# Optimization experiments

Hardware: AMD Instinct MI355X
Metric: run time of the kernel (lower is better)

The kernel has to match this reference:

```python
import jax, jax.numpy as jnp
import numpy as np

RATIO, NH, NG, KS, RF, UP = 4, 2, 2, 3, 11.0, 2


def _cln(t, g, b):
    # channel-wise LayerNorm on NCHW (LayerNormProxy), eps=1e-5
    mu = t.mean(axis=1, keepdims=True)
    var = ((t - mu) ** 2).mean(axis=1, keepdims=True)
    return (t - mu) * jax.lax.rsqrt(var + 1e-5) * g[None, :, None, None] + b[None, :, None, None]


def _resize_ac(img, oH, oW):
    # bilinear resize, align_corners=True (F.interpolate)
    H, W = img.shape[-2], img.shape[-1]
    ys = jnp.arange(oH, dtype=img.dtype) * ((H - 1) / (oH - 1))
    y0 = jnp.clip(jnp.floor(ys), 0, H - 2).astype(jnp.int32)
    wy = ys - y0.astype(img.dtype)
    xs = jnp.arange(oW, dtype=img.dtype) * ((W - 1) / (oW - 1))
    x0 = jnp.clip(jnp.floor(xs), 0, W - 2).astype(jnp.int32)
    wx = xs - x0.astype(img.dtype)
    t = img[..., y0, :] * (1.0 - wy)[:, None] + img[..., y0 + 1, :] * wy[:, None]
    return t[..., x0] * (1.0 - wx) + t[..., x0 + 1] * wx


def _grid_sample(img, iy, ix):
    # bilinear grid_sample, padding_mode='zeros', align_corners=True
    # img [Bg,Cx,H,W]; iy,ix [Bg,N] unnormalized input-pixel coords
    H, W = img.shape[-2], img.shape[-1]
    def one(im, yy, xx):
        y0f, x0f = jnp.floor(yy), jnp.floor(xx)
        wy, wx = yy - y0f, xx - x0f
        y0, x0 = y0f.astype(jnp.int32), x0f.astype(jnp.int32)
        def gat(yi, xi):
            valid = ((yi >= 0) & (yi < H) & (xi >= 0) & (xi < W)).astype(im.dtype)
            return im[:, jnp.clip(yi, 0, H - 1), jnp.clip(xi, 0, W - 1)] * valid[None]
        return (gat(y0, x0) * ((1 - wy) * (1 - wx))[None]
                + gat(y0, x0 + 1) * ((1 - wy) * wx)[None]
                + gat(y0 + 1, x0) * (wy * (1 - wx))[None]
                + gat(y0 + 1, x0 + 1) * (wy * wx)[None])
    return jax.vmap(one)(img, iy, ix)


def _conv2d(x, w, groups=1):
    return jax.lax.conv_general_dilated(x, w, (1, 1), 'SAME', feature_group_count=groups,
                                        dimension_numbers=('NCHW', 'OIHW', 'NCHW'))


def _forward(x, ln_g, ln_b, Wq, Wk, dw_w, off_ln_g, off_ln_b, off_w, off_b, rpb):
    B, C, H, W = x.shape
    hidden = C // RATIO
    gc = hidden // NG
    c2 = hidden // NH          # attn_dim per head
    oH, oW = int(H * UP), int(W * UP)
    N1, n = oH * oW, KS * KS
    scale = c2 ** -0.5
    v = x
    xn = _cln(x, ln_g, ln_b)
    q = jnp.einsum('oc,bchw->bohw', Wq, xn)
    k = jnp.einsum('oc,bchw->bohw', Wk, xn)
    q = _resize_ac(q, oH, oW)                        # [B,hidden,oH,oW]
    # offset prediction
    q_off = q.reshape(B * NG, gc, oH, oW)
    t = _conv2d(q_off, dw_w, groups=gc)
    t = _cln(t, off_ln_g, off_ln_b)
    t = jax.nn.gelu(t, approximate=False)
    pred = _conv2d(t, off_w) + off_b[None, :, None, None]  # [Bg,2*ks^2,oH,oW]
    pad = (KS - 1) // 2
    rng = jnp.arange(-pad, pad + 1, dtype=x.dtype)
    base = jnp.stack(jnp.meshgrid(rng, rng, indexing='ij'), axis=-1)  # [KS,KS,2] (y,x)
    off = jnp.tanh(pred).reshape(B * NG, KS, KS, 2, oH, oW) * RF + base[None, :, :, :, None, None]
    py = off[:, :, :, 0] + jnp.arange(oH, dtype=x.dtype)[None, None, None, :, None]
    px = off[:, :, :, 1] + jnp.arange(oW, dtype=x.dtype)[None, None, None, None, :]
    # normalize over (oH-1,oW-1) then denormalize onto (H-1,W-1) input grid (align_corners)
    iy = (py * ((H - 1) / (oH - 1))).reshape(B * NG, -1)
    ix = (px * ((W - 1) / (oW - 1))).reshape(B * NG, -1)
    kg = k.reshape(B * NG, hidden // NG, H, W)
    vg = v.reshape(B * NG, C // NG, H, W)
    kf = _grid_sample(kg, iy, ix).reshape(B, NG, hidden // NG, n, oH, oW)
    vf = _grid_sample(vg, iy, ix).reshape(B, NG, C // NG, n, oH, oW)
    # -> [B, N1, n, g*c] -> [B, nh, N1, n, c]
    kf = kf.transpose(0, 4, 5, 3, 1, 2).reshape(B, N1, n, NH, hidden // NH).transpose(0, 3, 1, 2, 4)
    vf = vf.transpose(0, 4, 5, 3, 1, 2).reshape(B, N1, n, NH, C // NH).transpose(0, 3, 1, 2, 4)
    kf = kf + rpb                                     # relative position bias on K
    qh = q.reshape(B, NH, c2, N1).transpose(0, 1, 3, 2) * scale  # [B,nh,N1,c2]
    attn = jax.nn.softmax(jnp.einsum('bhnc,bhnkc->bhnk', qh, kf), axis=-1)
    out = jnp.einsum('bhnk,bhnkc->bhnc', attn, vf)    # [B,nh,N1,C/nh]
    return out.transpose(0, 1, 3, 2).reshape(B, C, oH, oW)


def setup_inputs() -> dict:
    key = jax.random.key(0)
    ks = jax.random.split(key, 8)
    B, C, H, W = 2, 256, 48, 48
    hidden = C // RATIO
    gc = hidden // NG
    c2 = hidden // NH
    f32 = jnp.float32
    return {
        'x': jax.random.normal(ks[0], (B, C, H, W), f32),
        'ln_g': jnp.ones((C,), f32),
        'ln_b': jnp.zeros((C,), f32),
        'Wq': jax.random.normal(ks[1], (hidden, C), f32) * 0.05,
        'Wk': jax.random.normal(ks[2], (hidden, C), f32) * 0.05,
        'dw_w': jax.random.normal(ks[3], (gc, 1, 3, 3), f32) * 0.1,
        'off_ln_g': jnp.ones((gc,), f32),
        'off_ln_b': jnp.zeros((gc,), f32),
        'off_w': jax.random.normal(ks[4], (2 * KS * KS, gc, 3, 3), f32) * 0.02,
        'off_b': jnp.zeros((2 * KS * KS,), f32),
        'rpb': jax.random.normal(ks[5], (1, NH, 1, KS * KS, c2), f32) * 0.02,
    }


def reference(x, ln_g, ln_b, Wq, Wk, dw_w, off_ln_g, off_ln_b, off_w, off_b, rpb):
    return _forward(x, ln_g, ln_b, Wq, Wk, dw_w, off_ln_g, off_ln_b, off_w, off_b, rpb)
```

## Files before the change

### kernel.cpp

```cpp
#include <hip/hip_runtime.h>
#include <cstdint>
#include <cmath>

#define NB 2
#define NC 256
#define HW 2304
#define HID 64
#define OH 96
#define OW 96
#define N1 9216
#define SCALE_ATTN 0.17677669529663689f
#define RESZ ((float)(47.0/95.0))

__global__ void kA_prep(const float* __restrict__ x, const float* __restrict__ Wq,
                        const float* __restrict__ Wk, const float* __restrict__ off_w,
                        float* __restrict__ v_nhwc, float* __restrict__ WT4,
                        float* __restrict__ wT2) {
    int blk = blockIdx.x;
    if (blk < 1152) {
        int pt = blk % 72;
        int t2 = blk / 72;
        int ct = t2 & 3;
        int bg = t2 >> 2;
        int b = bg >> 1, g = bg & 1;
        __shared__ float tile[32][33];
        int tx = threadIdx.x & 31, row = threadIdx.x >> 5;
#pragma unroll
        for (int r = 0; r < 4; r++) {
            int c = ct * 32 + row + r * 8;
            tile[row + r * 8][tx] = x[((size_t)(b * 256 + g * 128 + c)) * HW + pt * 32 + tx];
        }
        __syncthreads();
#pragma unroll
        for (int r = 0; r < 4; r++) {
            int p = pt * 32 + row + r * 8;
            v_nhwc[((size_t)bg * HW + p) * 128 + ct * 32 + tx] = tile[tx][row + r * 8];
        }
    } else {
        int idx = (blk - 1152) * 256 + threadIdx.x;
        if (idx < 256 * 128) {
            int c = idx >> 7, t = idx & 127;
            float v = (t < 64) ? Wq[t * 256 + c] : Wk[(t - 64) * 256 + c];
            WT4[(((size_t)(c >> 2) * 128) + t) * 4 + (c & 3)] = v;
        } else if (idx < 256 * 128 + 288 * 18) {
            int i = idx - 256 * 128;
            wT2[i] = off_w[(i % 18) * 288 + (i / 18)];
        }
    }
}

__global__ __launch_bounds__(256) void k1_ln_qk(const float* __restrict__ v_nhwc,
                         const float* __restrict__ ln_g, const float* __restrict__ ln_b,
                         const float* __restrict__ WT4,
                         float* __restrict__ q_pix, float* __restrict__ k_nhwc) {
    int blk = blockIdx.x;
    int tid = threadIdx.x;
    int wv = tid >> 6, lane = tid & 63;
    __shared__ float xs[4][256];
    {
        int pix = blk * 4 + wv;
        int b = pix / HW, p = pix % HW;
        int c0 = lane * 2;
        float2 u0 = *(const float2*)(v_nhwc + (((size_t)(b * 2 + 0) * HW) + p) * 128 + c0);
        float2 u1 = *(const float2*)(v_nhwc + (((size_t)(b * 2 + 1) * HW) + p) * 128 + c0);
        float s = u0.x + u0.y + u1.x + u1.y;
#pragma unroll
        for (int off = 1; off < 64; off <<= 1) s += __shfl_xor(s, off);
        float mu = s * (1.f / 256.f);
        float d0 = u0.x - mu, d1 = u0.y - mu, d2 = u1.x - mu, d3 = u1.y - mu;
        float q = d0 * d0 + d1 * d1 + d2 * d2 + d3 * d3;
#pragma unroll
        for (int off = 1; off < 64; off <<= 1) q += __shfl_xor(q, off);
        float rs = rsqrtf(q * (1.f / 256.f) + 1e-5f);
        float2 w0, w1;
        w0.x = d0 * rs * ln_g[c0] + ln_b[c0];
        w0.y = d1 * rs * ln_g[c0 + 1] + ln_b[c0 + 1];
        w1.x = d2 * rs * ln_g[128 + c0] + ln_b[128 + c0];
        w1.y = d3 * rs * ln_g[129 + c0] + ln_b[129 + c0];
        *(float2*)&xs[wv][c0] = w0;
        *(float2*)&xs[wv][128 + c0] = w1;
    }
    __syncthreads();
    int o = tid & 127, ph = tid >> 7;
    float a0 = 0.f, a1 = 0.f;
    const float4* wp = (const float4*)WT4 + o;
    const float4* xa = (const float4*)xs[ph * 2];
    const float4* xb = (const float4*)xs[ph * 2 + 1];
#pragma unroll 8
    for (int c4 = 0; c4 < 64; c4++) {
        float4 w = wp[(size_t)c4 * 128];
        float4 p0 = xa[c4], p1 = xb[c4];
        a0 += w.x * p0.x + w.y * p0.y + w.z * p0.z + w.w * p0.w;
        a1 += w.x * p1.x + w.y * p1.y + w.z * p1.z + w.w * p1.w;
    }
#pragma unroll
    for (int k = 0; k < 2; k++) {
        int pix = blk * 4 + ph * 2 + k;
        int b = pix / HW, p = pix % HW;
        float a = k ? a1 : a0;
        if (o < 64) {
            q_pix[(((size_t)b * HW) + p) * 64 + o] = a;
        } else {
            int t = o - 64, g = t >> 5, c32 = t & 31;
            k_nhwc[(((size_t)(b * 2 + g) * HW) + p) * 32 + c32] = a;
        }
    }
}

__global__ __launch_bounds__(256) void k34_off(const float* __restrict__ q_pix,
                                               const float* __restrict__ dw_w,
                                               const float* __restrict__ og,
                                               const float* __restrict__ ob,
                                               const float* __restrict__ wT2,
                                               const float* __restrict__ off_b,
                                               float* __restrict__ pred) {
    int blk = blockIdx.x;
    int bg = blk / 72, tile = blk % 72;
    int ty0 = (tile / 6) * 8, tx0 = (tile % 6) * 16;
    int b = bg >> 1, g = bg & 1;
    int tid = threadIdx.x;
    __shared__ float ts[180][33];

    if (tid < 180) {
        int hy = ty0 + tid / 18 - 1;
        int hx = tx0 + tid % 18 - 1;
        if (hy < 0 || hy >= OH || hx < 0 || hx >= OW) {
#pragma unroll
            for (int c = 0; c < 32; c++) ts[tid][c] = 0.f;
        } else {
            const float* qb = q_pix + (size_t)b * HW * 64 + g * 32;
            float vals[32];
#pragma unroll
            for (int c = 0; c < 32; c++) vals[c] = 0.f;
            for (int dy = -1; dy <= 1; dy++) {
                int yy = hy + dy;
                if ((unsigned)yy >= (unsigned)OH) continue;
                float ysf = yy * RESZ;
                int y0 = min((int)ysf, 46);
                float wy = ysf - (float)y0;
                for (int dx = -1; dx <= 1; dx++) {
                    int xx = hx + dx;
                    if ((unsigned)xx >= (unsigned)OW) continue;
                    float xsf = xx * RESZ;
                    int x0 = min((int)xsf, 46);
                    float wx = xsf - (float)x0;
                    int i00 = (y0 * 48 + x0) * 64;
                    const float4* q00 = (const float4*)(qb + i00);
                    const float4* q01 = (const float4*)(qb + i00 + 64);
                    const float4* q10 = (const float4*)(qb + i00 + 48 * 64);
                    const float4* q11 = (const float4*)(qb + i00 + 49 * 64);
                    float w00 = (1.f - wy) * (1.f - wx), w01 = (1.f - wy) * wx;
                    float w10 = wy * (1.f - wx),         w11 = wy * wx;
                    int wi = (dy + 1) * 3 + (dx + 1);
#pragma unroll
                    for (int c4 = 0; c4 < 8; c4++) {
                        float4 a = q00[c4], bq = q01[c4], cq = q10[c4], dq = q11[c4];
                        float qx = w00 * a.x + w01 * bq.x + w10 * cq.x + w11 * dq.x;
                        float qy = w00 * a.y + w01 * bq.y + w10 * cq.y + w11 * dq.y;
                        float qz = w00 * a.z + w01 * bq.z + w10 * cq.z + w11 * dq.z;
                        float qw = w00 * a.w + w01 * bq.w + w10 * cq.w + w11 * dq.w;
                        vals[c4 * 4 + 0] += qx * dw_w[(c4 * 4 + 0) * 9 + wi];
                        vals[c4 * 4 + 1] += qy * dw_w[(c4 * 4 + 1) * 9 + wi];
                        vals[c4 * 4 + 2] += qz * dw_w[(c4 * 4 + 2) * 9 + wi];
                        vals[c4 * 4 + 3] += qw * dw_w[(c4 * 4 + 3) * 9 + wi];
                    }
                }
            }
            float sum = 0.f;
#pragma unroll
            for (int c = 0; c < 32; c++) sum += vals[c];
            float mu = sum * (1.f / 32.f);
            float var = 0.f;
#pragma unroll
            for (int c = 0; c < 32; c++) { float d = vals[c] - mu; var += d * d; }
            float rsv = rsqrtf(var * (1.f / 32.f) + 1e-5f);
#pragma unroll
            for (int c = 0; c < 32; c++) {
                float v = (vals[c] - mu) * rsv * og[c] + ob[c];
                ts[tid][c] = 0.5f * v * (1.f + erff(v * 0.70710678118654752f));
            }
        }
    }
    __syncthreads();

    int och = __builtin_amdgcn_readfirstlane(tid >> 7) * 9;
    int pixL = tid & 127;
    int oyl = pixL >> 4, oxl = pixL & 15;
    float acc[9];
#pragma unroll
    for (int o = 0; o < 9; o++) acc[o] = off_b[och + o];
    for (int ic = 0; ic < 32; ic++) {
#pragma unroll
        for (int dy = 0; dy < 3; dy++) {
#pragma unroll
            for (int dx = 0; dx < 3; dx++) {
                float tv = ts[(oyl + dy) * 18 + oxl + dx][ic];
                const float* wr = wT2 + (ic * 9 + dy * 3 + dx) * 18 + och;
#pragma unroll
                for (int o = 0; o < 9; o++) acc[o] += tv * wr[o];
            }
        }
    }
    int p = (ty0 + oyl) * OW + tx0 + oxl;
#pragma unroll
    for (int o = 0; o < 9; o++)
        pred[((size_t)bg * 18 + och + o) * N1 + p] = acc[o];
}

__global__ __launch_bounds__(256) void k5_attn(const float* __restrict__ pred,
                                               const float* __restrict__ q_pix,
                                               const float* __restrict__ k_nhwc,
                                               const float* __restrict__ v_nhwc,
                                               const float* __restrict__ rpb,
                                               float* __restrict__ out) {
    int tid = threadIdx.x;
    int wv = __builtin_amdgcn_readfirstlane(tid >> 6);
    int lane = tid & 63;
    int gp = blockIdx.x * 16;
    int bg = gp / N1, p0 = gp % N1;
    int b = bg >> 1, g = bg & 1;
    int pw = p0 + wv * 4;
    int oy = pw / OW, ox0 = pw % OW;

    __shared__ float4 wts[4][4][9];
    __shared__ int4   cof[4][4][9];
    __shared__ float  outb[4][4][128];

    if (lane < 36) {
        int px = lane / 9, j = lane % 9;
        int p = pw + px;
        int ky = j / 3, kx = j % 3;
        float pr0 = pred[((size_t)bg * 18 + j * 2) * N1 + p];
        float pr1 = pred[((size_t)bg * 18 + j * 2 + 1) * N1 + p];
        float th0 = 1.f - 2.f * __builtin_amdgcn_rcpf(__expf(2.f * pr0) + 1.f);
        float th1 = 1.f - 2.f * __builtin_amdgcn_rcpf(__expf(2.f * pr1) + 1.f);
        float py  = th0 * 11.0f + (float)(ky - 1) + (float)oy;
        float pxc = th1 * 11.0f + (float)(kx - 1) + (float)(ox0 + px);
        float iy = py * RESZ, ix = pxc * RESZ;
        float y0f = floorf(iy), x0f = floorf(ix);
        float wy = iy - y0f, wx = ix - x0f;
        int y0 = (int)y0f, x0 = (int)x0f;
        bool vy0 = (unsigned)y0 < 48u, vy1 = (unsigned)(y0 + 1) < 48u;
        bool vx0 = (unsigned)x0 < 48u, vx1 = (unsigned)(x0 + 1) < 48u;
        int y0c = min(max(y0, 0), 47), y1c = min(max(y0 + 1, 0), 47);
        int x0c = min(max(x0, 0), 47), x1c = min(max(x0 + 1, 0), 47);
        float4 w;
        w.x = (vy0 && vx0) ? (1.f - wy) * (1.f - wx) : 0.f;
        w.y = (vy0 && vx1) ? (1.f - wy) * wx : 0.f;
        w.z = (vy1 && vx0) ? wy * (1.f - wx) : 0.f;
        w.w = (vy1 && vx1) ? wy * wx : 0.f;
        wts[wv][px][j] = w;
        cof[wv][px][j] = make_int4(y0c * 48 + x0c, y0c * 48 + x1c,
                                   y1c * 48 + x0c, y1c * 48 + x1c);
    }
    __syncthreads();

    int c = lane & 31, h = lane >> 5;
    int c4 = (lane & 31) * 4;
    const float* kb = k_nhwc + (size_t)bg * HW * 32;
    const float* rb = rpb + (size_t)g * 288;
    const float* qb = q_pix + (size_t)b * HW * 64 + g * 32 + c;
    const float* vbase = v_nhwc + (size_t)bg * HW * 128;

    float ysf = oy * RESZ;
    int qy0 = min((int)ysf, 46);
    float qwy = ysf - (float)qy0;

    for (int px = 0; px < 4; px++) {
        float xsf = (ox0 + px) * RESZ;
        int qx0 = min((int)xsf, 46);
        float qwx = xsf - (float)qx0;
        int qi = (qy0 * 48 + qx0) * 64;
        float q00 = qb[qi], q01 = qb[qi + 64];
        float q10 = qb[qi + 48 * 64], q11 = qb[qi + 49 * 64];
        float qv = ((q00 * (1.f - qwy) + q10 * qwy) * (1.f - qwx)
                  + (q01 * (1.f - qwy) + q11 * qwy) * qwx) * SCALE_ATTN;

        float s[5], e[5];
#pragma unroll
        for (int jj = 0; jj < 5; jj++) {
            int j = jj * 2 + h;
            float partial = 0.f;
            if (j < 9) {
                float4 w = wts[wv][px][j];
                int4 co = cof[wv][px][j];
                float kv = w.x * kb[co.x * 32 + c] + w.y * kb[co.y * 32 + c]
                         + w.z * kb[co.z * 32 + c] + w.w * kb[co.w * 32 + c];
                partial = qv * (kv + rb[j * 32 + c]);
            }
#pragma unroll
            for (int off = 1; off < 32; off <<= 1) partial += __shfl_xor(partial, off);
            s[jj] = (j < 9) ? partial : -1e30f;
        }
        float m = s[0];
#pragma unroll
        for (int jj = 1; jj < 5; jj++) m = fmaxf(m, s[jj]);
        m = fmaxf(m, __shfl_xor(m, 32));
        float sum = 0.f;
#pragma unroll
        for (int jj = 0; jj < 5; jj++) { e[jj] = __expf(s[jj] - m); sum += e[jj]; }
        sum += __shfl_xor(sum, 32);
        float inv = __builtin_amdgcn_rcpf(sum);

        float4 acc = make_float4(0.f, 0.f, 0.f, 0.f);
#pragma unroll
        for (int jj = 0; jj < 5; jj++) {
            int j = jj * 2 + h;
            if (j < 9) {
                float pj = e[jj] * inv;
                float4 w = wts[wv][px][j];
                int4 co = cof[wv][px][j];
                float4 a0 = *(const float4*)(vbase + (size_t)co.x * 128 + c4);
                float4 a1 = *(const float4*)(vbase + (size_t)co.y * 128 + c4);
                float4 a2 = *(const float4*)(vbase + (size_t)co.z * 128 + c4);
                float4 a3 = *(const float4*)(vbase + (size_t)co.w * 128 + c4);
                float f0 = w.x * pj, f1 = w.y * pj, f2 = w.z * pj, f3 = w.w * pj;
                acc.x += f0 * a0.x + f1 * a1.x + f2 * a2.x + f3 * a3.x;
                acc.y += f0 * a0.y + f1 * a1.y + f2 * a2.y + f3 * a3.y;
                acc.z += f0 * a0.z + f1 * a1.z + f2 * a2.z + f3 * a3.z;
                acc.w += f0 * a0.w + f1 * a1.w + f2 * a2.w + f3 * a3.w;
            }
        }
        acc.x += __shfl_xor(acc.x, 32);
        acc.y += __shfl_xor(acc.y, 32);
        acc.z += __shfl_xor(acc.z, 32);
        acc.w += __shfl_xor(acc.w, 32);
        if (lane < 32) *(float4*)&outb[wv][px][c4] = acc;
    }
    __syncthreads();

    if (tid < 128) {
        int ch = tid;
        float* op = out + ((size_t)b * NC + g * 128 + ch) * N1 + p0;
#pragma unroll
        for (int w2 = 0; w2 < 4; w2++) {
            float4 v4 = make_float4(outb[w2][0][ch], outb[w2][1][ch],
                                    outb[w2][2][ch], outb[w2][3][ch]);
            *(float4*)(op + w2 * 4) = v4;
        }
    }
}

extern "C" void kernel_launch(void* const* d_in, const int* in_sizes, int n_in,
                              void* d_out, int out_size, void* d_ws, size_t ws_size,
                              hipStream_t stream) {
    const float* x      = (const float*)d_in[0];
    const float* ln_g   = (const float*)d_in[1];
    const float* ln_b   = (const float*)d_in[2];
    const float* Wq     = (const float*)d_in[3];
    const float* Wk     = (const float*)d_in[4];
    const float* dw_w   = (const float*)d_in[5];
    const float* off_g  = (const float*)d_in[6];
    const float* off_bt = (const float*)d_in[7];
    const float* off_w  = (const float*)d_in[8];
    const float* off_b  = (const float*)d_in[9];
    const float* rpb    = (const float*)d_in[10];
    float* out = (float*)d_out;

    float* ws = (float*)d_ws;
    float* WT4    = ws;
    float* k_nhwc = WT4 + 32768;
    float* v_nhwc = k_nhwc + 294912;
    float* q_pix  = v_nhwc + 1179648;
    float* pred   = q_pix + 294912;
    float* wT2    = pred + 663552;

    kA_prep<<<1301, 256, 0, stream>>>(x, Wq, Wk, off_w, v_nhwc, WT4, wT2);
    k1_ln_qk<<<1152, 256, 0, stream>>>(v_nhwc, ln_g, ln_b, WT4, q_pix, k_nhwc);
    k34_off<<<288, 256, 0, stream>>>(q_pix, dw_w, off_g, off_bt, wT2, off_b, pred);
    k5_attn<<<2304, 256, 0, stream>>>(pred, q_pix, k_nhwc, v_nhwc, rpb, out);
}
```

Baseline: 187.4 us.

## Split offset-network kernel into per-channel and per-output-channel kernels, reorder transpose

The fused k34_off kernel, which had only 288 blocks and heavy per-thread register arrays, is replaced by two high-parallelism kernels. k3_t computes the upsampled depthwise conv, LayerNorm and GELU with one thread per channel per pixel, using wave shuffles for the reductions. k4_pred computes the 3x3 offset conv with one thread per output channel per pixel, writing pred in pixel-major layout. The QK LayerNorm now reads x directly in NCHW instead of the transposed copy, and the v transpose runs later so it can reuse the buffer that held tbuf. This is meant to raise occupancy and parallelism at the cost of an extra intermediate buffer round trip through global memory and more redundant neighbour reads in k4.

```diff
diff --git a/kernel.cpp b/kernel.cpp
--- a/kernel.cpp
+++ b/kernel.cpp
@@ -12,44 +12,26 @@
 #define SCALE_ATTN 0.17677669529663689f
 #define RESZ ((float)(47.0/95.0))
 
-__global__ void kA_prep(const float* __restrict__ x, const float* __restrict__ Wq,
-                        const float* __restrict__ Wk, const float* __restrict__ off_w,
-                        float* __restrict__ v_nhwc, float* __restrict__ WT4,
-                        float* __restrict__ wT2) {
-    int blk = blockIdx.x;
-    if (blk < 1152) {
-        int pt = blk % 72;
-        int t2 = blk / 72;
-        int ct = t2 & 3;
-        int bg = t2 >> 2;
-        int b = bg >> 1, g = bg & 1;
-        __shared__ float tile[32][33];
-        int tx = threadIdx.x & 31, row = threadIdx.x >> 5;
-#pragma unroll
-        for (int r = 0; r < 4; r++) {
-            int c = ct * 32 + row + r * 8;
-            tile[row + r * 8][tx] = x[((size_t)(b * 256 + g * 128 + c)) * HW + pt * 32 + tx];
-        }
-        __syncthreads();
-#pragma unroll
-        for (int r = 0; r < 4; r++) {
-            int p = pt * 32 + row + r * 8;
-            v_nhwc[((size_t)bg * HW + p) * 128 + ct * 32 + tx] = tile[tx][row + r * 8];
-        }
-    } else {
-        int idx = (blk - 1152) * 256 + threadIdx.x;
-        if (idx < 256 * 128) {
-            int c = idx >> 7, t = idx & 127;
-            float v = (t < 64) ? Wq[t * 256 + c] : Wk[(t - 64) * 256 + c];
-            WT4[(((size_t)(c >> 2) * 128) + t) * 4 + (c & 3)] = v;
-        } else if (idx < 256 * 128 + 288 * 18) {
-            int i = idx - 256 * 128;
-            wT2[i] = off_w[(i % 18) * 288 + (i / 18)];
-        }
-    }
-}
-
-__global__ __launch_bounds__(256) void k1_ln_qk(const float* __restrict__ v_nhwc,
+__global__ void kA_prep(const float* __restrict__ Wq, const float* __restrict__ Wk,
+                        const float* __restrict__ off_w, const float* __restrict__ dw_w,
+                        float* __restrict__ WT4, float* __restrict__ wT2,
+                        float* __restrict__ dwT) {
+    int idx = blockIdx.x * 256 + threadIdx.x;
+    if (idx < 256 * 128) {
+        int c = idx >> 7, t = idx & 127;
+        float v = (t < 64) ? Wq[t * 256 + c] : Wk[(t - 64) * 256 + c];
+        WT4[(((size_t)(c >> 2) * 128) + t) * 4 + (c & 3)] = v;
+    } else if (idx < 256 * 128 + 288 * 18) {
+        int i = idx - 256 * 128;
+        wT2[i] = off_w[(i % 18) * 288 + (i / 18)];
+    } else if (idx < 256 * 128 + 288 * 18 + 288) {
+        int i = idx - (256 * 128 + 288 * 18);
+        int wi = i >> 5, c = i & 31;
+        dwT[i] = dw_w[c * 9 + wi];
+    }
+}
+
+__global__ __launch_bounds__(256) void k1_ln_qk(const float* __restrict__ x,
                          const float* __restrict__ ln_g, const float* __restrict__ ln_b,
                          const float* __restrict__ WT4,
                          float* __restrict__ q_pix, float* __restrict__ k_nhwc) {
@@ -59,44 +41,43 @@
     __shared__ float xs[4][256];
     {
         int pix = blk * 4 + wv;
-        int b = pix / HW, p = pix % HW;
-        int c0 = lane * 2;
-        float2 u0 = *(const float2*)(v_nhwc + (((size_t)(b * 2 + 0) * HW) + p) * 128 + c0);
-        float2 u1 = *(const float2*)(v_nhwc + (((size_t)(b * 2 + 1) * HW) + p) * 128 + c0);
-        float s = u0.x + u0.y + u1.x + u1.y;
+        int b = pix / HW, p = pix - b * HW;
+        const float* xb = x + (size_t)b * NC * HW + p;
+        float v0 = xb[(size_t)lane * HW];
+        float v1 = xb[(size_t)(lane + 64) * HW];
+        float v2 = xb[(size_t)(lane + 128) * HW];
+        float v3 = xb[(size_t)(lane + 192) * HW];
+        float s = v0 + v1 + v2 + v3;
 #pragma unroll
         for (int off = 1; off < 64; off <<= 1) s += __shfl_xor(s, off);
         float mu = s * (1.f / 256.f);
-        float d0 = u0.x - mu, d1 = u0.y - mu, d2 = u1.x - mu, d3 = u1.y - mu;
+        float d0 = v0 - mu, d1 = v1 - mu, d2 = v2 - mu, d3 = v3 - mu;
         float q = d0 * d0 + d1 * d1 + d2 * d2 + d3 * d3;
 #pragma unroll
         for (int off = 1; off < 64; off <<= 1) q += __shfl_xor(q, off);
         float rs = rsqrtf(q * (1.f / 256.f) + 1e-5f);
-        float2 w0, w1;
-        w0.x = d0 * rs * ln_g[c0] + ln_b[c0];
-        w0.y = d1 * rs * ln_g[c0 + 1] + ln_b[c0 + 1];
-        w1.x = d2 * rs * ln_g[128 + c0] + ln_b[128 + c0];
-        w1.y = d3 * rs * ln_g[129 + c0] + ln_b[129 + c0];
-        *(float2*)&xs[wv][c0] = w0;
-        *(float2*)&xs[wv][128 + c0] = w1;
+        xs[wv][lane]       = d0 * rs * ln_g[lane]       + ln_b[lane];
+        xs[wv][lane + 64]  = d1 * rs * ln_g[lane + 64]  + ln_b[lane + 64];
+        xs[wv][lane + 128] = d2 * rs * ln_g[lane + 128] + ln_b[lane + 128];
+        xs[wv][lane + 192] = d3 * rs * ln_g[lane + 192] + ln_b[lane + 192];
     }
     __syncthreads();
     int o = tid & 127, ph = tid >> 7;
     float a0 = 0.f, a1 = 0.f;
     const float4* wp = (const float4*)WT4 + o;
     const float4* xa = (const float4*)xs[ph * 2];
-    const float4* xb = (const float4*)xs[ph * 2 + 1];
+    const float4* xb4 = (const float4*)xs[ph * 2 + 1];
 #pragma unroll 8
     for (int c4 = 0; c4 < 64; c4++) {
         float4 w = wp[(size_t)c4 * 128];
-        float4 p0 = xa[c4], p1 = xb[c4];
+        float4 p0 = xa[c4], p1 = xb4[c4];
         a0 += w.x * p0.x + w.y * p0.y + w.z * p0.z + w.w * p0.w;
         a1 += w.x * p1.x + w.y * p1.y + w.z * p1.z + w.w * p1.w;
     }
 #pragma unroll
     for (int k = 0; k < 2; k++) {
         int pix = blk * 4 + ph * 2 + k;
-        int b = pix / HW, p = pix % HW;
+        int b = pix / HW, p = pix - b * HW;
         float a = k ? a1 : a0;
         if (o < 64) {
             q_pix[(((size_t)b * HW) + p) * 64 + o] = a;
@@ -107,104 +88,105 @@
     }
 }
 
-__global__ __launch_bounds__(256) void k34_off(const float* __restrict__ q_pix,
-                                               const float* __restrict__ dw_w,
-                                               const float* __restrict__ og,
-                                               const float* __restrict__ ob,
+__global__ __launch_bounds__(256) void k3_t(const float* __restrict__ q_pix,
+                                            const float* __restrict__ dwT,
+                                            const float* __restrict__ og,
+                                            const float* __restrict__ ob,
+                                            float* __restrict__ tbuf) {
+    int gid = blockIdx.x * 256 + threadIdx.x;
+    int c = gid & 31;
+    int p2 = gid >> 5;
+    int bg = p2 / N1, p = p2 - bg * N1;
+    int b = bg >> 1, g = bg & 1;
+    int oy = p / OW, ox = p - oy * OW;
+    const float* qb = q_pix + ((size_t)b * HW) * 64 + g * 32 + c;
+    float acc = 0.f;
+#pragma unroll
+    for (int dy = -1; dy <= 1; dy++) {
+        int yy = oy + dy;
+        if ((unsigned)yy >= (unsigned)OH) continue;
+        float ysf = yy * RESZ;
+        int y0 = min((int)ysf, 46);
+        float wy = ysf - (float)y0;
+#pragma unroll
+        for (int dx = -1; dx <= 1; dx++) {
+            int xx = ox + dx;
+            if ((unsigned)xx >= (unsigned)OW) continue;
+            float xsf = xx * RESZ;
+            int x0 = min((int)xsf, 46);
+            float wx = xsf - (float)x0;
+            int i00 = (y0 * 48 + x0) * 64;
+            float q00 = qb[i00], q01 = qb[i00 + 64];
+            float q10 = qb[i00 + 48 * 64], q11 = qb[i00 + 49 * 64];
+            float qv = (q00 * (1.f - wy) + q10 * wy) * (1.f - wx)
+                     + (q01 * (1.f - wy) + q11 * wy) * wx;
+            acc += qv * dwT[((dy + 1) * 3 + dx + 1) * 32 + c];
+        }
+    }
+    float s = acc;
+#pragma unroll
+    for (int off = 1; off < 32; off <<= 1) s += __shfl_xor(s, off);
+    float mu = s * (1.f / 32.f);
+    float d = acc - mu;
+    float v = d * d;
+#pragma unroll
+    for (int off = 1; off < 32; off <<= 1) v += __shfl_xor(v, off);
+    float rsv = rsqrtf(v * (1.f / 32.f) + 1e-5f);
+    float t = d * rsv * og[c] + ob[c];
+    float ge = 0.5f * t * (1.f + erff(t * 0.70710678118654752f));
+    tbuf[(size_t)p2 * 32 + c] = ge;
+}
+
+__global__ __launch_bounds__(256) void k4_pred(const float* __restrict__ tbuf,
                                                const float* __restrict__ wT2,
                                                const float* __restrict__ off_b,
                                                float* __restrict__ pred) {
+    int gid = blockIdx.x * 256 + threadIdx.x;
+    if (gid >= 4 * N1 * 18) return;
+    int p18 = gid / 18, oc = gid - p18 * 18;
+    int bg = p18 / N1, p = p18 - bg * N1;
+    int oy = p / OW, ox = p - oy * OW;
+    const float* tb = tbuf + (size_t)bg * N1 * 32;
+    int pn[9];
+    bool vl[9];
+#pragma unroll
+    for (int dy = -1; dy <= 1; dy++)
+#pragma unroll
+        for (int dx = -1; dx <= 1; dx++) {
+            int k = (dy + 1) * 3 + (dx + 1);
+            vl[k] = ((unsigned)(oy + dy) < (unsigned)OH) && ((unsigned)(ox + dx) < (unsigned)OW);
+            pn[k] = (p + dy * OW + dx) * 32;
+        }
+    float acc = off_b[oc];
+    for (int ic = 0; ic < 32; ic++) {
+#pragma unroll
+        for (int k = 0; k < 9; k++) {
+            if (vl[k]) acc += tb[pn[k] + ic] * wT2[(ic * 9 + k) * 18 + oc];
+        }
+    }
+    pred[gid] = acc;
+}
+
+__global__ void k2b_vt(const float* __restrict__ x, float* __restrict__ v_nhwc) {
     int blk = blockIdx.x;
-    int bg = blk / 72, tile = blk % 72;
-    int ty0 = (tile / 6) * 8, tx0 = (tile % 6) * 16;
+    int pt = blk % 72;
+    int t2 = blk / 72;
+    int ct = t2 & 3;
+    int bg = t2 >> 2;
     int b = bg >> 1, g = bg & 1;
-    int tid = threadIdx.x;
-    __shared__ float ts[180][33];
-
-    if (tid < 180) {
-        int hy = ty0 + tid / 18 - 1;
-        int hx = tx0 + tid % 18 - 1;
-        if (hy < 0 || hy >= OH || hx < 0 || hx >= OW) {
-#pragma unroll
-            for (int c = 0; c < 32; c++) ts[tid][c] = 0.f;
-        } else {
-            const float* qb = q_pix + (size_t)b * HW * 64 + g * 32;
-            float vals[32];
-#pragma unroll
-            for (int c = 0; c < 32; c++) vals[c] = 0.f;
-            for (int dy = -1; dy <= 1; dy++) {
-                int yy = hy + dy;
-                if ((unsigned)yy >= (unsigned)OH) continue;
-                float ysf = yy * RESZ;
-                int y0 = min((int)ysf, 46);
-                float wy = ysf - (float)y0;
-                for (int dx = -1; dx <= 1; dx++) {
-                    int xx = hx + dx;
-                    if ((unsigned)xx >= (unsigned)OW) continue;
-                    float xsf = xx * RESZ;
-                    int x0 = min((int)xsf, 46);
-                    float wx = xsf - (float)x0;
-                    int i00 = (y0 * 48 + x0) * 64;
-                    const float4* q00 = (const float4*)(qb + i00);
-                    const float4* q01 = (const float4*)(qb + i00 + 64);
-                    const float4* q10 = (const float4*)(qb + i00 + 48 * 64);
-                    const float4* q11 = (const float4*)(qb + i00 + 49 * 64);
-                    float w00 = (1.f - wy) * (1.f - wx), w01 = (1.f - wy) * wx;
-                    float w10 = wy * (1.f - wx),         w11 = wy * wx;
-                    int wi = (dy + 1) * 3 + (dx + 1);
-#pragma unroll
-                    for (int c4 = 0; c4 < 8; c4++) {
-                        float4 a = q00[c4], bq = q01[c4], cq = q10[c4], dq = q11[c4];
-                        float qx = w00 * a.x + w01 * bq.x + w10 * cq.x + w11 * dq.x;
-                        float qy = w00 * a.y + w01 * bq.y + w10 * cq.y + w11 * dq.y;
-                        float qz = w00 * a.z + w01 * bq.z + w10 * cq.z + w11 * dq.z;
-                        float qw = w00 * a.w + w01 * bq.w + w10 * cq.w + w11 * dq.w;
-                        vals[c4 * 4 + 0] += qx * dw_w[(c4 * 4 + 0) * 9 + wi];
-                        vals[c4 * 4 + 1] += qy * dw_w[(c4 * 4 + 1) * 9 + wi];
-                        vals[c4 * 4 + 2] += qz * dw_w[(c4 * 4 + 2) * 9 + wi];
-                        vals[c4 * 4 + 3] += qw * dw_w[(c4 * 4 + 3) * 9 + wi];
-                    }
-                }
-            }
-            float sum = 0.f;
-#pragma unroll
-            for (int c = 0; c < 32; c++) sum += vals[c];
-            float mu = sum * (1.f / 32.f);
-            float var = 0.f;
-#pragma unroll
-            for (int c = 0; c < 32; c++) { float d = vals[c] - mu; var += d * d; }
-            float rsv = rsqrtf(var * (1.f / 32.f) + 1e-5f);
-#pragma unroll
-            for (int c = 0; c < 32; c++) {
-                float v = (vals[c] - mu) * rsv * og[c] + ob[c];
-                ts[tid][c] = 0.5f * v * (1.f + erff(v * 0.70710678118654752f));
-            }
-        }
+    __shared__ float tile[32][33];
+    int tx = threadIdx.x & 31, row = threadIdx.x >> 5;
+#pragma unroll
+    for (int r = 0; r < 4; r++) {
+        int c = ct * 32 + row + r * 8;
+        tile[row + r * 8][tx] = x[((size_t)(b * 256 + g * 128 + c)) * HW + pt * 32 + tx];
     }
     __syncthreads();
-
-    int och = __builtin_amdgcn_readfirstlane(tid >> 7) * 9;
-    int pixL = tid & 127;
-    int oyl = pixL >> 4, oxl = pixL & 15;
-    float acc[9];
-#pragma unroll
-    for (int o = 0; o < 9; o++) acc[o] = off_b[och + o];
-    for (int ic = 0; ic < 32; ic++) {
-#pragma unroll
-        for (int dy = 0; dy < 3; dy++) {
-#pragma unroll
-            for (int dx = 0; dx < 3; dx++) {
-                float tv = ts[(oyl + dy) * 18 + oxl + dx][ic];
-                const float* wr = wT2 + (ic * 9 + dy * 3 + dx) * 18 + och;
-#pragma unroll
-                for (int o = 0; o < 9; o++) acc[o] += tv * wr[o];
-            }
-        }
-    }
-    int p = (ty0 + oyl) * OW + tx0 + oxl;
-#pragma unroll
-    for (int o = 0; o < 9; o++)
-        pred[((size_t)bg * 18 + och + o) * N1 + p] = acc[o];
+#pragma unroll
+    for (int r = 0; r < 4; r++) {
+        int p = pt * 32 + row + r * 8;
+        v_nhwc[((size_t)bg * HW + p) * 128 + ct * 32 + tx] = tile[tx][row + r * 8];
+    }
 }
 
 __global__ __launch_bounds__(256) void k5_attn(const float* __restrict__ pred,
@@ -230,8 +212,9 @@
         int px = lane / 9, j = lane % 9;
         int p = pw + px;
         int ky = j / 3, kx = j % 3;
-        float pr0 = pred[((size_t)bg * 18 + j * 2) * N1 + p];
-        float pr1 = pred[((size_t)bg * 18 + j * 2 + 1) * N1 + p];
+        const float* pp = pred + ((size_t)bg * N1 + p) * 18;
+        float pr0 = pp[j * 2];
+        float pr1 = pp[j * 2 + 1];
         float th0 = 1.f - 2.f * __builtin_amdgcn_rcpf(__expf(2.f * pr0) + 1.f);
         float th1 = 1.f - 2.f * __builtin_amdgcn_rcpf(__expf(2.f * pr1) + 1.f);
         float py  = th0 * 11.0f + (float)(ky - 1) + (float)oy;
@@ -358,15 +341,20 @@
     float* out = (float*)d_out;
 
     float* ws = (float*)d_ws;
-    float* WT4    = ws;
+    float* U      = ws;
+    float* tbuf   = U;
+    float* v_nhwc = U;
+    float* WT4    = U + 1179648;
     float* k_nhwc = WT4 + 32768;
-    float* v_nhwc = k_nhwc + 294912;
-    float* q_pix  = v_nhwc + 1179648;
+    float* q_pix  = k_nhwc + 294912;
     float* pred   = q_pix + 294912;
     float* wT2    = pred + 663552;
-
-    kA_prep<<<1301, 256, 0, stream>>>(x, Wq, Wk, off_w, v_nhwc, WT4, wT2);
-    k1_ln_qk<<<1152, 256, 0, stream>>>(v_nhwc, ln_g, ln_b, WT4, q_pix, k_nhwc);
-    k34_off<<<288, 256, 0, stream>>>(q_pix, dw_w, off_g, off_bt, wT2, off_b, pred);
+    float* dwT    = wT2 + 5184;
+
+    kA_prep<<<150, 256, 0, stream>>>(Wq, Wk, off_w, dw_w, WT4, wT2, dwT);
+    k1_ln_qk<<<1152, 256, 0, stream>>>(x, ln_g, ln_b, WT4, q_pix, k_nhwc);
+    k3_t<<<4608, 256, 0, stream>>>(q_pix, dwT, off_g, off_bt, tbuf);
+    k4_pred<<<2592, 256, 0, stream>>>(tbuf, wT2, off_b, pred);
+    k2b_vt<<<1152, 256, 0, stream>>>(x, v_nhwc);
     k5_attn<<<2304, 256, 0, stream>>>(pred, q_pix, k_nhwc, v_nhwc, rpb, out);
 }
```

After: 356.5 us. 1.9x slower.
